# Performance work log

Hardware: AMD Instinct MI355X
Metric: run time of the kernel (lower is better)

The kernel has to match this reference:

```python
import jax, jax.numpy as jnp
import numpy as np

# db8 decomposition low-pass filter (pywt ordering, dec_lo)
_DB8_DEC_LO = np.array([
    -0.00011747678400228192, 0.0006754494059985568, -0.0003917403729959771,
    -0.00487035299301066, 0.008746094047015655, 0.013981027917015516,
    -0.04408825393106472, -0.01736930100202211, 0.128747426620186,
    0.00047248457399797254, -0.2840155429624281, -0.015829105256023893,
    0.5853546836548691, 0.6756307362980128, 0.3128715909144659,
    0.05441584224308161], dtype=np.float32)
_F = len(_DB8_DEC_LO)  # 16 taps
# quadrature mirror relation used by pywt: dec_hi[k] = (-1)^(k+1) * dec_lo[F-1-k]
_DB8_DEC_HI = (((-1.0) ** (np.arange(_F) + 1)) * _DB8_DEC_LO[::-1]).astype(np.float32)
# lax conv is cross-correlation; np.convolve flips the kernel -> pre-flip filters.
# Kernel layout [out_ch=2 (lo,hi), in_ch=1, width=F]
_KERNEL = jnp.asarray(np.stack([_DB8_DEC_LO[::-1], _DB8_DEC_HI[::-1]])[:, None, :])

WAVELET_LEVEL = 3
SPECTRAL_WEIGHT = 1.0
WAVELET_WEIGHT = 1.0


def _dwt_level(x):
    """Single-level db8 DWT with pywt 'symmetric' padding, batched over rows.

    x: [N, L] -> (cA, cD) each [N, (L + F - 1) // 2]
    Matches: np.convolve(sym_pad(x, F-1), dec_filter, 'valid')[1::2]
    """
    p = _F - 1
    # half-sample symmetric extension: [x_p..x_1 | x | x_{L-1}..x_{L-p}]
    xe = jnp.concatenate([x[:, :p][:, ::-1], x, x[:, -p:][:, ::-1]], axis=1)
    xe = xe[:, 1:]  # start at odd offset to mimic pywt's [1::2] downsampling
    out = jax.lax.conv_general_dilated(
        xe[:, None, :], _KERNEL, window_strides=(2,), padding='VALID')  # [N,2,Lc]
    return out[:, 0, :], out[:, 1, :]


def _wavelet_loss(output, target, level):
    """Batched equivalent of the per-row pywt.wavedec loop: MSE on detail
    subbands at every level, averaged over (rows x levels)."""
    b, c, H, W = output.shape
    x = output.reshape(b * c * H, W)
    y = target.reshape(b * c * H, W)
    total = jnp.float32(0.0)
    for _ in range(level):  # fixed small loop over decomposition levels
        x, dx = _dwt_level(x)
        y, dy = _dwt_level(y)
        total = total + jnp.mean((dx - dy) ** 2)
    return total / level


def setup_inputs() -> dict:
    key = jax.random.key(0)
    k1, k2 = jax.random.split(key)
    shape = (32, 1, 1024, 1024)
    output = jax.random.normal(k1, shape, dtype=jnp.float32)
    target = jax.random.normal(k2, shape, dtype=jnp.float32)
    return {"output": output, "target": target}


def reference(output, target):
    # MSE term
    mse = jnp.mean((output - target) ** 2)
    # spectral second-difference smoothness along wavelength axis (last dim)
    sd = output[:, :, :, 2:] - 2.0 * output[:, :, :, 1:-1] + output[:, :, :, :-2]
    spectral = jnp.mean(sd ** 2)
    # original wavelet loss detaches inputs (numpy path) -> no gradient
    wavelet = _wavelet_loss(jax.lax.stop_gradient(output),
                            jax.lax.stop_gradient(target), WAVELET_LEVEL)
    return mse + SPECTRAL_WEIGHT * spectral + WAVELET_WEIGHT * wavelet
```

## Files before the change

### kernel.cpp

```cpp
#include <hip/hip_runtime.h>

#define NROWS 32768
#define NBLK  8192

typedef _Float16 h2 __attribute__((ext_vector_type(2)));

#define H2C(a,b) {(_Float16)(a##f), (_Float16)(b##f)}

__device__ __forceinline__ float DOT2(unsigned w, h2 f, float acc) {
#if __has_builtin(__builtin_amdgcn_fdot2)
    return __builtin_amdgcn_fdot2(__builtin_bit_cast(h2, w), f, acc, false);
#else
    h2 v = __builtin_bit_cast(h2, w);
    return fmaf((float)v.y, (float)f.y, fmaf((float)v.x, (float)f.x, acc));
#endif
}

__device__ __forceinline__ unsigned PK(float lo, float hi) {
    return __builtin_bit_cast(unsigned, __builtin_amdgcn_cvt_pkrtz(lo, hi));
}

__device__ __forceinline__ unsigned ROR16(unsigned v) { return (v >> 16) | (v << 16); }

__device__ __forceinline__ void wave_lgkm0() {
    asm volatile("s_waitcnt lgkmcnt(0)" ::: "memory");
}

template<int M, bool STORE>
__device__ __forceinline__ float level_group(const unsigned* __restrict__ inb,
                                             unsigned* __restrict__ outb, int g)
{
    constexpr h2 FA[8] = {
        H2C(0.05441584224308161, 0.3128715909144659),
        H2C(0.6756307362980128, 0.5853546836548691),
        H2C(-0.015829105256023893, -0.2840155429624281),
        H2C(0.00047248457399797254, 0.128747426620186),
        H2C(-0.01736930100202211, -0.04408825393106472),
        H2C(0.013981027917015516, 0.008746094047015655),
        H2C(-0.00487035299301066, -0.0003917403729959771),
        H2C(0.0006754494059985568, -0.00011747678400228192)
    };
    constexpr h2 FD[8] = {
        H2C(-0.00011747678400228192, -0.0006754494059985568),
        H2C(-0.0003917403729959771, 0.00487035299301066),
        H2C(0.008746094047015655, -0.013981027917015516),
        H2C(-0.04408825393106472, 0.01736930100202211),
        H2C(0.128747426620186, -0.00047248457399797254),
        H2C(-0.2840155429624281, 0.015829105256023893),
        H2C(0.5853546836548691, -0.6756307362980128),
        H2C(0.3128715909144659, -0.05441584224308161)
    };
    const uint4 q0 = *(const uint4*)(inb + 4 * g);
    const uint4 q1 = *(const uint4*)(inb + 4 * g + 4);
    const uint4 q2 = *(const uint4*)(inb + 4 * g + 8);
    const unsigned w[12] = {q0.x,q0.y,q0.z,q0.w, q1.x,q1.y,q1.z,q1.w, q2.x,q2.y,q2.z,q2.w};

    float aj[4] = {0.f,0.f,0.f,0.f}, dj[4] = {0.f,0.f,0.f,0.f};
#pragma unroll
    for (int c = 0; c < 8; ++c) {
#pragma unroll
        for (int j = 0; j < 4; ++j) {
            aj[j] = DOT2(w[j+1+c], FA[c], aj[j]);
            dj[j] = DOT2(w[j+1+c], FD[c], dj[j]);
        }
    }
    const int i0 = 4 * g;
    float ds = dj[0] * dj[0];
    if (i0 + 1 < M) ds += dj[1] * dj[1];
    if (i0 + 2 < M) ds += dj[2] * dj[2];
    if (i0 + 3 < M) ds += dj[3] * dj[3];
    if (STORE) {
        *(uint2*)(outb + 8 + 2 * g) = make_uint2(PK(aj[0], aj[1]), PK(aj[2], aj[3]));
    }
    return ds;
}

__device__ __forceinline__ void fix_front(unsigned* b, int lane) {
    if (lane < 7) b[7 - lane] = ROR16(b[8 + lane]);
}
__device__ __forceinline__ void fix_tail_even(unsigned* b, int lane, int HL) {
    if (lane < 7) b[8 + HL + lane] = ROR16(b[8 + HL - 1 - lane]);
}
__device__ __forceinline__ void fix_tail_odd(unsigned* b, int lane, int q) {
    if (lane < 7) b[8 + q + 1 + lane] = ROR16(b[8 + q - 1 - lane]);
    if (lane == 7) { unsigned v = b[8 + q]; b[8 + q] = (v & 0xffffu) | (v << 16); }
}

__global__ __launch_bounds__(256) void combined_loss_kernel(
    const float* __restrict__ x, const float* __restrict__ y,
    float* __restrict__ partials)
{
    __shared__ __align__(16) unsigned lds[4][956];
    __shared__ float wsum[4];

    const int tid  = threadIdx.x;
    const int wid  = tid >> 6;
    const int lane = tid & 63;
    unsigned* const W  = lds[wid];
    unsigned* const B0 = W;
    unsigned* const B1 = W + 528;
    unsigned* const B2 = W + 804;

    const int row = blockIdx.x * 4 + wid;
    const float4* xp = (const float4*)x + (size_t)row * 256;
    const float4* yp = (const float4*)y + (size_t)row * 256;

    float4 xc[4];
    float s_mse = 0.f, s_spec = 0.f;

#pragma unroll
    for (int c = 0; c < 4; ++c) {
        const float4 xv = xp[c * 64 + lane];
        const float4 yv = yp[c * 64 + lane];
        xc[c] = xv;
        const float4 ev = make_float4(xv.x - yv.x, xv.y - yv.y, xv.z - yv.z, xv.w - yv.w);
        s_mse += ev.x * ev.x + ev.y * ev.y + ev.z * ev.z + ev.w * ev.w;
        const int u = c * 64 + lane;
        *(uint2*)(B0 + 8 + 2 * u) = make_uint2(PK(ev.x, ev.y), PK(ev.z, ev.w));
    }

#pragma unroll
    for (int c = 0; c < 4; ++c) {
        const float4 xv = xc[c];
        float n0 = __shfl_down(xv.x, 1, 64);
        float n1 = __shfl_down(xv.y, 1, 64);
        if (c < 3) {
            const float b0 = __shfl(xc[c + 1].x, 0, 64);
            const float b1 = __shfl(xc[c + 1].y, 0, 64);
            if (lane == 63) { n0 = b0; n1 = b1; }
        }
        const float sd0 = xv.x - 2.f * xv.y + xv.z;
        const float sd1 = xv.y - 2.f * xv.z + xv.w;
        s_spec += sd0 * sd0 + sd1 * sd1;
        const float sd2 = xv.z - 2.f * xv.w + n0;
        const float sd3 = xv.w - 2.f * n0 + n1;
        if (c < 3 || lane < 63)
            s_spec += sd2 * sd2 + sd3 * sd3;
    }

    float s_d1 = 0.f, s_d2 = 0.f, s_d3 = 0.f;

    wave_lgkm0();
    fix_front(B0, lane); fix_tail_even(B0, lane, 512);
    wave_lgkm0();

    for (int g = lane; g < 130; g += 64) s_d1 += level_group<519, true>(B0, B1, g);
    wave_lgkm0();
    fix_front(B1, lane); fix_tail_odd(B1, lane, 259);
    wave_lgkm0();

    for (int g = lane; g < 67; g += 64)  s_d2 += level_group<267, true>(B1, B2, g);
    wave_lgkm0();
    fix_front(B2, lane); fix_tail_odd(B2, lane, 133);
    wave_lgkm0();

    if (lane < 36)                       s_d3 += level_group<141, false>(B2, B2, lane);

    const float wm  = 1.0f / 33554432.0f;
    const float wsp = 1.0f / 33488896.0f;
    const float w1  = 1.0f / (3.0f * 17006592.0f);
    const float w2  = 1.0f / (3.0f * 8749056.0f);
    const float w3  = 1.0f / (3.0f * 4620288.0f);
    float local = wm * s_mse + wsp * s_spec + w1 * s_d1 + w2 * s_d2 + w3 * s_d3;

#pragma unroll
    for (int off = 32; off > 0; off >>= 1)
        local += __shfl_down(local, off, 64);
    if (lane == 0) wsum[wid] = local;
    __syncthreads();
    if (tid == 0) partials[blockIdx.x] = wsum[0] + wsum[1] + wsum[2] + wsum[3];
}

__global__ __launch_bounds__(256) void reduce_kernel(const float* __restrict__ partials,
                                                     int n, float* __restrict__ out)
{
    __shared__ double sm[256];
    double s = 0.0;
    for (int i = threadIdx.x; i < n; i += 256) s += (double)partials[i];
    sm[threadIdx.x] = s;
    __syncthreads();
    for (int off = 128; off > 0; off >>= 1) {
        if (threadIdx.x < off) sm[threadIdx.x] += sm[threadIdx.x + off];
        __syncthreads();
    }
    if (threadIdx.x == 0) out[0] = (float)sm[0];
}

extern "C" void kernel_launch(void* const* d_in, const int* in_sizes, int n_in,
                              void* d_out, int out_size, void* d_ws, size_t ws_size,
                              hipStream_t stream) {
    const float* x = (const float*)d_in[0];
    const float* y = (const float*)d_in[1];
    float* partials = (float*)d_ws;
    combined_loss_kernel<<<NBLK, 256, 0, stream>>>(x, y, partials);
    reduce_kernel<<<1, 256, 0, stream>>>(partials, NBLK, (float*)d_out);
}
```

Baseline: 55.23 us.

## Process two rows per wavefront and pack wavelet groups across rows

Each wavefront now handles two rows instead of one, so the grid halves and LDS doubles per block. All eight float4 loads per lane are issued together before any arithmetic, which raises memory-level parallelism. The DWT group loops for the two rows are merged, so lanes that sat idle at levels 2 and 3 now do work, and the boundary fix-ups for both rows run on disjoint lane ranges. Costs are more registers and LDS per block, which may lower occupancy.

```diff
diff --git a/kernel.cpp b/kernel.cpp
--- a/kernel.cpp
+++ b/kernel.cpp
@@ -1,7 +1,7 @@
 #include <hip/hip_runtime.h>
 
 #define NROWS 32768
-#define NBLK  8192
+#define NBLK  4096
 
 typedef _Float16 h2 __attribute__((ext_vector_type(2)));
 
@@ -75,50 +75,19 @@
     return ds;
 }
 
-__device__ __forceinline__ void fix_front(unsigned* b, int lane) {
-    if (lane < 7) b[7 - lane] = ROR16(b[8 + lane]);
-}
-__device__ __forceinline__ void fix_tail_even(unsigned* b, int lane, int HL) {
-    if (lane < 7) b[8 + HL + lane] = ROR16(b[8 + HL - 1 - lane]);
-}
-__device__ __forceinline__ void fix_tail_odd(unsigned* b, int lane, int q) {
-    if (lane < 7) b[8 + q + 1 + lane] = ROR16(b[8 + q - 1 - lane]);
-    if (lane == 7) { unsigned v = b[8 + q]; b[8 + q] = (v & 0xffffu) | (v << 16); }
-}
-
-__global__ __launch_bounds__(256) void combined_loss_kernel(
-    const float* __restrict__ x, const float* __restrict__ y,
-    float* __restrict__ partials)
-{
-    __shared__ __align__(16) unsigned lds[4][956];
-    __shared__ float wsum[4];
-
-    const int tid  = threadIdx.x;
-    const int wid  = tid >> 6;
-    const int lane = tid & 63;
-    unsigned* const W  = lds[wid];
-    unsigned* const B0 = W;
-    unsigned* const B1 = W + 528;
-    unsigned* const B2 = W + 804;
-
-    const int row = blockIdx.x * 4 + wid;
-    const float4* xp = (const float4*)x + (size_t)row * 256;
-    const float4* yp = (const float4*)y + (size_t)row * 256;
-
-    float4 xc[4];
-    float s_mse = 0.f, s_spec = 0.f;
-
-#pragma unroll
-    for (int c = 0; c < 4; ++c) {
-        const float4 xv = xp[c * 64 + lane];
-        const float4 yv = yp[c * 64 + lane];
-        xc[c] = xv;
-        const float4 ev = make_float4(xv.x - yv.x, xv.y - yv.y, xv.z - yv.z, xv.w - yv.w);
-        s_mse += ev.x * ev.x + ev.y * ev.y + ev.z * ev.z + ev.w * ev.w;
-        const int u = c * 64 + lane;
-        *(uint2*)(B0 + 8 + 2 * u) = make_uint2(PK(ev.x, ev.y), PK(ev.z, ev.w));
-    }
-
+__device__ __forceinline__ void fix_front(unsigned* b, int l) {
+    if ((unsigned)l < 7u) b[7 - l] = ROR16(b[8 + l]);
+}
+__device__ __forceinline__ void fix_tail_even(unsigned* b, int l, int HL) {
+    if ((unsigned)l < 7u) b[8 + HL + l] = ROR16(b[8 + HL - 1 - l]);
+}
+__device__ __forceinline__ void fix_tail_odd(unsigned* b, int l, int q) {
+    if ((unsigned)l < 7u) b[8 + q + 1 + l] = ROR16(b[8 + q - 1 - l]);
+    if (l == 7) { unsigned v = b[8 + q]; b[8 + q] = (v & 0xffffu) | (v << 16); }
+}
+
+__device__ __forceinline__ float spectral_row(const float4* xc, int lane) {
+    float s = 0.f;
 #pragma unroll
     for (int c = 0; c < 4; ++c) {
         const float4 xv = xc[c];
@@ -131,30 +100,93 @@
         }
         const float sd0 = xv.x - 2.f * xv.y + xv.z;
         const float sd1 = xv.y - 2.f * xv.z + xv.w;
-        s_spec += sd0 * sd0 + sd1 * sd1;
+        s += sd0 * sd0 + sd1 * sd1;
         const float sd2 = xv.z - 2.f * xv.w + n0;
         const float sd3 = xv.w - 2.f * n0 + n1;
         if (c < 3 || lane < 63)
-            s_spec += sd2 * sd2 + sd3 * sd3;
-    }
+            s += sd2 * sd2 + sd3 * sd3;
+    }
+    return s;
+}
+
+__global__ __launch_bounds__(256) void combined_loss_kernel(
+    const float* __restrict__ x, const float* __restrict__ y,
+    float* __restrict__ partials)
+{
+    __shared__ __align__(16) unsigned lds[8][956];
+    __shared__ float wsum[4];
+
+    const int tid  = threadIdx.x;
+    const int wid  = tid >> 6;
+    const int lane = tid & 63;
+    unsigned* const W0 = lds[wid * 2];
+    unsigned* const W1 = lds[wid * 2 + 1];
+
+    const int row0 = (blockIdx.x * 4 + wid) * 2;
+    const float4* xp0 = (const float4*)x + (size_t)row0 * 256;
+    const float4* yp0 = (const float4*)y + (size_t)row0 * 256;
+    const float4* xp1 = xp0 + 256;
+    const float4* yp1 = yp0 + 256;
+
+    float4 x0[4], y0[4], x1[4], y1[4];
+#pragma unroll
+    for (int c = 0; c < 4; ++c) {
+        x0[c] = xp0[c * 64 + lane];  y0[c] = yp0[c * 64 + lane];
+        x1[c] = xp1[c * 64 + lane];  y1[c] = yp1[c * 64 + lane];
+    }
+
+    float s_mse = 0.f, s_spec = 0.f;
+#pragma unroll
+    for (int c = 0; c < 4; ++c) {
+        const int u = c * 64 + lane;
+        const float4 e0 = make_float4(x0[c].x - y0[c].x, x0[c].y - y0[c].y,
+                                      x0[c].z - y0[c].z, x0[c].w - y0[c].w);
+        s_mse += e0.x * e0.x + e0.y * e0.y + e0.z * e0.z + e0.w * e0.w;
+        *(uint2*)(W0 + 8 + 2 * u) = make_uint2(PK(e0.x, e0.y), PK(e0.z, e0.w));
+        const float4 e1 = make_float4(x1[c].x - y1[c].x, x1[c].y - y1[c].y,
+                                      x1[c].z - y1[c].z, x1[c].w - y1[c].w);
+        s_mse += e1.x * e1.x + e1.y * e1.y + e1.z * e1.z + e1.w * e1.w;
+        *(uint2*)(W1 + 8 + 2 * u) = make_uint2(PK(e1.x, e1.y), PK(e1.z, e1.w));
+    }
+
+    s_spec += spectral_row(x0, lane);
+    s_spec += spectral_row(x1, lane);
 
     float s_d1 = 0.f, s_d2 = 0.f, s_d3 = 0.f;
 
     wave_lgkm0();
-    fix_front(B0, lane); fix_tail_even(B0, lane, 512);
-    wave_lgkm0();
-
-    for (int g = lane; g < 130; g += 64) s_d1 += level_group<519, true>(B0, B1, g);
-    wave_lgkm0();
-    fix_front(B1, lane); fix_tail_odd(B1, lane, 259);
-    wave_lgkm0();
-
-    for (int g = lane; g < 67; g += 64)  s_d2 += level_group<267, true>(B1, B2, g);
-    wave_lgkm0();
-    fix_front(B2, lane); fix_tail_odd(B2, lane, 133);
-    wave_lgkm0();
-
-    if (lane < 36)                       s_d3 += level_group<141, false>(B2, B2, lane);
+    fix_front(W0, lane);      fix_tail_even(W0, lane - 16, 512);
+    fix_front(W1, lane - 32); fix_tail_even(W1, lane - 48, 512);
+    wave_lgkm0();
+
+    for (int g = lane; g < 260; g += 64) {
+        const int r = g >= 130;
+        const int gg = g - (r ? 130 : 0);
+        unsigned* const W = r ? W1 : W0;
+        s_d1 += level_group<519, true>(W, W + 528, gg);
+    }
+    wave_lgkm0();
+    fix_front(W0 + 528, lane);      fix_tail_odd(W0 + 528, lane - 16, 259);
+    fix_front(W1 + 528, lane - 32); fix_tail_odd(W1 + 528, lane - 48, 259);
+    wave_lgkm0();
+
+    for (int g = lane; g < 134; g += 64) {
+        const int r = g >= 67;
+        const int gg = g - (r ? 67 : 0);
+        unsigned* const W = r ? W1 : W0;
+        s_d2 += level_group<267, true>(W + 528, W + 804, gg);
+    }
+    wave_lgkm0();
+    fix_front(W0 + 804, lane);      fix_tail_odd(W0 + 804, lane - 16, 133);
+    fix_front(W1 + 804, lane - 32); fix_tail_odd(W1 + 804, lane - 48, 133);
+    wave_lgkm0();
+
+    for (int g = lane; g < 72; g += 64) {
+        const int r = g >= 36;
+        const int gg = g - (r ? 36 : 0);
+        unsigned* const W = r ? W1 : W0;
+        s_d3 += level_group<141, false>(W + 804, W + 804, gg);
+    }
 
     const float wm  = 1.0f / 33554432.0f;
     const float wsp = 1.0f / 33488896.0f;
```

New measurement: 54.46 us. Within noise of the previous version (-1.4%).

## Process four rows per wave with software-prefetched next-row loads

Applied to the files above, without the earlier changes.

Each wave now handles four consecutive rows instead of one, cutting the grid to a quarter as many blocks. The next row's x and y loads are issued before the wavelet stages of the current row, so global-memory latency overlaps the LDS-bound DWT work. The front and tail boundary fixups now run on different lane ranges so they can execute in parallel. In exchange there are fewer waves to hide latency, more live registers for the prefetched data, and a serial per-wave loop.

```diff
diff --git a/kernel.cpp b/kernel.cpp
--- a/kernel.cpp
+++ b/kernel.cpp
@@ -1,7 +1,8 @@
 #include <hip/hip_runtime.h>
 
 #define NROWS 32768
-#define NBLK  8192
+#define NBLK  2048
+#define RPW   4
 
 typedef _Float16 h2 __attribute__((ext_vector_type(2)));
 
@@ -75,50 +76,19 @@
     return ds;
 }
 
-__device__ __forceinline__ void fix_front(unsigned* b, int lane) {
-    if (lane < 7) b[7 - lane] = ROR16(b[8 + lane]);
-}
-__device__ __forceinline__ void fix_tail_even(unsigned* b, int lane, int HL) {
-    if (lane < 7) b[8 + HL + lane] = ROR16(b[8 + HL - 1 - lane]);
-}
-__device__ __forceinline__ void fix_tail_odd(unsigned* b, int lane, int q) {
-    if (lane < 7) b[8 + q + 1 + lane] = ROR16(b[8 + q - 1 - lane]);
-    if (lane == 7) { unsigned v = b[8 + q]; b[8 + q] = (v & 0xffffu) | (v << 16); }
-}
-
-__global__ __launch_bounds__(256) void combined_loss_kernel(
-    const float* __restrict__ x, const float* __restrict__ y,
-    float* __restrict__ partials)
-{
-    __shared__ __align__(16) unsigned lds[4][956];
-    __shared__ float wsum[4];
-
-    const int tid  = threadIdx.x;
-    const int wid  = tid >> 6;
-    const int lane = tid & 63;
-    unsigned* const W  = lds[wid];
-    unsigned* const B0 = W;
-    unsigned* const B1 = W + 528;
-    unsigned* const B2 = W + 804;
-
-    const int row = blockIdx.x * 4 + wid;
-    const float4* xp = (const float4*)x + (size_t)row * 256;
-    const float4* yp = (const float4*)y + (size_t)row * 256;
-
-    float4 xc[4];
-    float s_mse = 0.f, s_spec = 0.f;
-
-#pragma unroll
-    for (int c = 0; c < 4; ++c) {
-        const float4 xv = xp[c * 64 + lane];
-        const float4 yv = yp[c * 64 + lane];
-        xc[c] = xv;
-        const float4 ev = make_float4(xv.x - yv.x, xv.y - yv.y, xv.z - yv.z, xv.w - yv.w);
-        s_mse += ev.x * ev.x + ev.y * ev.y + ev.z * ev.z + ev.w * ev.w;
-        const int u = c * 64 + lane;
-        *(uint2*)(B0 + 8 + 2 * u) = make_uint2(PK(ev.x, ev.y), PK(ev.z, ev.w));
-    }
-
+__device__ __forceinline__ void fix_front(unsigned* b, int l) {
+    if ((unsigned)l < 7u) b[7 - l] = ROR16(b[8 + l]);
+}
+__device__ __forceinline__ void fix_tail_even(unsigned* b, int l, int HL) {
+    if ((unsigned)l < 7u) b[8 + HL + l] = ROR16(b[8 + HL - 1 - l]);
+}
+__device__ __forceinline__ void fix_tail_odd(unsigned* b, int l, int q) {
+    if ((unsigned)l < 7u) b[8 + q + 1 + l] = ROR16(b[8 + q - 1 - l]);
+    if (l == 7) { unsigned v = b[8 + q]; b[8 + q] = (v & 0xffffu) | (v << 16); }
+}
+
+__device__ __forceinline__ float spectral_row(const float4* xc, int lane) {
+    float s = 0.f;
 #pragma unroll
     for (int c = 0; c < 4; ++c) {
         const float4 xv = xc[c];
@@ -131,30 +101,78 @@
         }
         const float sd0 = xv.x - 2.f * xv.y + xv.z;
         const float sd1 = xv.y - 2.f * xv.z + xv.w;
-        s_spec += sd0 * sd0 + sd1 * sd1;
+        s += sd0 * sd0 + sd1 * sd1;
         const float sd2 = xv.z - 2.f * xv.w + n0;
         const float sd3 = xv.w - 2.f * n0 + n1;
         if (c < 3 || lane < 63)
-            s_spec += sd2 * sd2 + sd3 * sd3;
-    }
-
-    float s_d1 = 0.f, s_d2 = 0.f, s_d3 = 0.f;
-
-    wave_lgkm0();
-    fix_front(B0, lane); fix_tail_even(B0, lane, 512);
-    wave_lgkm0();
-
-    for (int g = lane; g < 130; g += 64) s_d1 += level_group<519, true>(B0, B1, g);
-    wave_lgkm0();
-    fix_front(B1, lane); fix_tail_odd(B1, lane, 259);
-    wave_lgkm0();
-
-    for (int g = lane; g < 67; g += 64)  s_d2 += level_group<267, true>(B1, B2, g);
-    wave_lgkm0();
-    fix_front(B2, lane); fix_tail_odd(B2, lane, 133);
-    wave_lgkm0();
-
-    if (lane < 36)                       s_d3 += level_group<141, false>(B2, B2, lane);
+            s += sd2 * sd2 + sd3 * sd3;
+    }
+    return s;
+}
+
+__global__ __launch_bounds__(256) void combined_loss_kernel(
+    const float* __restrict__ x, const float* __restrict__ y,
+    float* __restrict__ partials)
+{
+    __shared__ __align__(16) unsigned lds[4][956];
+    __shared__ float wsum[4];
+
+    const int tid  = threadIdx.x;
+    const int wid  = tid >> 6;
+    const int lane = tid & 63;
+    unsigned* const W  = lds[wid];
+    unsigned* const B0 = W;
+    unsigned* const B1 = W + 528;
+    unsigned* const B2 = W + 804;
+
+    const int rbase = (blockIdx.x * 4 + wid) * RPW;
+    const float4* xp = (const float4*)x + (size_t)rbase * 256;
+    const float4* yp = (const float4*)y + (size_t)rbase * 256;
+
+    float4 xc[4], yc[4];
+#pragma unroll
+    for (int c = 0; c < 4; ++c) {
+        xc[c] = xp[c * 64 + lane];
+        yc[c] = yp[c * 64 + lane];
+    }
+
+    float s_mse = 0.f, s_spec = 0.f, s_d1 = 0.f, s_d2 = 0.f, s_d3 = 0.f;
+
+#pragma unroll 1
+    for (int k = 0; k < RPW; ++k) {
+#pragma unroll
+        for (int c = 0; c < 4; ++c) {
+            const int u = c * 64 + lane;
+            const float4 e = make_float4(xc[c].x - yc[c].x, xc[c].y - yc[c].y,
+                                         xc[c].z - yc[c].z, xc[c].w - yc[c].w);
+            s_mse += e.x * e.x + e.y * e.y + e.z * e.z + e.w * e.w;
+            *(uint2*)(B0 + 8 + 2 * u) = make_uint2(PK(e.x, e.y), PK(e.z, e.w));
+        }
+        s_spec += spectral_row(xc, lane);
+
+        if (k + 1 < RPW) {
+            const float4* xpn = xp + (size_t)(k + 1) * 256;
+            const float4* ypn = yp + (size_t)(k + 1) * 256;
+#pragma unroll
+            for (int c = 0; c < 4; ++c) {
+                xc[c] = xpn[c * 64 + lane];
+                yc[c] = ypn[c * 64 + lane];
+            }
+        }
+
+        wave_lgkm0();
+        fix_front(B0, lane); fix_tail_even(B0, lane - 16, 512);
+        wave_lgkm0();
+        for (int g = lane; g < 130; g += 64) s_d1 += level_group<519, true>(B0, B1, g);
+        wave_lgkm0();
+        fix_front(B1, lane); fix_tail_odd(B1, lane - 16, 259);
+        wave_lgkm0();
+        for (int g = lane; g < 67; g += 64)  s_d2 += level_group<267, true>(B1, B2, g);
+        wave_lgkm0();
+        fix_front(B2, lane); fix_tail_odd(B2, lane - 16, 133);
+        wave_lgkm0();
+        if (lane < 36)                       s_d3 += level_group<141, false>(B2, B2, lane);
+    }
 
     const float wm  = 1.0f / 33554432.0f;
     const float wsp = 1.0f / 33488896.0f;
```

Result: no change. 54.29 us (-1.7%).
